# Performance work log

Measured on AMD Instinct MI355X. Metric: run time of the kernel, lower is better.

Reference implementation:

```python
import jax, jax.numpy as jnp
import numpy as np

N, T, D, H = 32, 512, 1024, 1024


def setup_inputs() -> dict:
    key = jax.random.key(0)
    k1, k2, k3, k4 = jax.random.split(key, 4)
    x = jax.random.normal(k1, (N, T, D), jnp.float32)
    prev_ht = jax.random.normal(k2, (N, H), jnp.float32)
    # scale weights to keep sigmoid/tanh out of hard saturation
    weight = jax.random.normal(k3, (D + H, 3 * (D + H)), jnp.float32) / np.sqrt(D + H).astype(np.float32)
    bias = jax.random.normal(k4, (3 * (D + H),), jnp.float32) * 0.1
    return {"x": x, "prev_ht": prev_ht, "weight": weight, "bias": bias}


def _gridgru_forward(x, prev_ht, weight, bias):
    # weight layout per get_weights()
    Wxt = weight[:D, :3 * H]          # (D, 3H)
    Wxd = weight[:D, 3 * H:]          # (D, 3D)
    Whd = weight[D:, 3 * H:]          # (H, 3D)
    Whtg = weight[D:, :2 * H]         # (H, 2H)
    Whtc = weight[D:, 2 * H:3 * H]    # (H, H)
    bt = bias[:3 * H]
    bd = bias[3 * H:]

    # input projection for temporal gates, done once: (N, T, 3H)
    gates = jnp.einsum('ntd,dk->ntk', x, Wxt) + bt

    # temporal GRU recurrence over T (zoneout=0, inference)
    def step(h, g):  # h: (N,H), g: (N,3H)
        gg = jax.nn.sigmoid(g[:, :2 * H] + h @ Whtg)
        u = gg[:, :H]
        r = gg[:, H:]
        hc = jnp.tanh(g[:, 2 * H:] + (r * h) @ Whtc)
        hn = h + u * (hc - h)  # = h - u*h + u*hc
        return hn, hn

    last_ht, ht_t = jax.lax.scan(step, prev_ht, jnp.swapaxes(gates, 0, 1))
    ht = jnp.swapaxes(ht_t, 0, 1)  # (N, T, H)

    # depth-wise gated recurrence (applied per-timestep, no sequential dep)
    grd = jax.nn.sigmoid(bd[:2 * D]
                         + jnp.einsum('ntd,de->nte', x, Wxd[:, :2 * D])
                         + jnp.einsum('nth,he->nte', ht, Whd[:, :2 * D]))
    ud = grd[..., :D]
    rd = grd[..., D:]
    hcd = jnp.tanh(bd[2 * D:]
                   + jnp.einsum('nth,he->nte', ht, Whd[:, 2 * D:])
                   + jnp.einsum('ntd,de->nte', rd * x, Wxd[:, 2 * D:]))
    h = x + ud * (hcd - x)  # = x - ud*x + ud*hcd
    return h, last_ht


def reference(x, prev_ht, weight, bias):
    return _gridgru_forward(x, prev_ht, weight, bias)
```

## Files before the change

### kernel.cpp

```cpp
#include <hip/hip_runtime.h>
#include <stdint.h>

#define T_STEPS 512

typedef short short8 __attribute__((ext_vector_type(8)));
typedef float floatx4 __attribute__((ext_vector_type(4)));
typedef unsigned int u32x4 __attribute__((ext_vector_type(4)));
typedef unsigned int u32x2 __attribute__((ext_vector_type(2)));

#define MFMA16 __builtin_amdgcn_mfma_f32_16x16x32_bf16

__device__ __forceinline__ unsigned short f2bf(float f) {
  unsigned int u = __builtin_bit_cast(unsigned int, f);
  u = u + 0x7fff + ((u >> 16) & 1);
  return (unsigned short)(u >> 16);
}
__device__ __forceinline__ float bf2f(unsigned short s) {
  unsigned int u = ((unsigned int)s) << 16;
  return __builtin_bit_cast(float, u);
}
__device__ __forceinline__ float sigm(float x) { return 1.f / (1.f + __expf(-x)); }
__device__ __forceinline__ float tanh_fast(float x) {
  float e2 = __expf(2.f * x);
  return 1.f - 2.f / (e2 + 1.f);
}

__device__ __forceinline__ void gload16(const void* g, const void* l) {
  __builtin_amdgcn_global_load_lds((const __attribute__((address_space(1))) unsigned int*)g,
                                   (__attribute__((address_space(3))) unsigned int*)l,
                                   16, 0, 0);
}

__device__ __forceinline__ void st_tag(unsigned int* p, unsigned int word) {
  asm volatile("global_store_dword %0, %1, off sc0 sc1" :: "v"(p), "v"(word) : "memory");
}

__device__ __forceinline__ void stage_state(const unsigned int* __restrict__ gsrc,
                                            unsigned int target,
                                            unsigned short* Stg, int tid) {
  const int lane = tid & 63, wave = tid >> 6;
  const unsigned int* src = gsrc + wave * 4096 + lane * 4;
  u32x4 w[16];
  int spins = 0;
  for (;;) {
#pragma unroll
    for (int j = 0; j < 16; ++j)
      asm volatile("global_load_dwordx4 %0, %1, off sc0 sc1"
                   : "=v"(w[j]) : "v"(src + j * 256));
    asm volatile("s_waitcnt vmcnt(0)" ::: "memory");
    __builtin_amdgcn_sched_barrier(0);
    bool ok = true;
#pragma unroll
    for (int j = 0; j < 16; ++j)
#pragma unroll
      for (int q = 0; q < 4; ++q) ok &= ((w[j][q] >> 16) >= target);
    if (__all((int)ok) || ++spins > (1 << 15)) break;
    if (spins > 4) __builtin_amdgcn_s_sleep(1);
  }
  const int half = lane & 1;
  const int chb = lane >> 1;
#pragma unroll
  for (int j = 0; j < 16; ++j) {
    int row = wave * 4 + (j >> 2);
    int c16 = (j & 3) * 32 + chb;
    u32x2 v;
    v[0] = (w[j][0] & 0xffffu) | (w[j][1] << 16);
    v[1] = (w[j][2] & 0xffffu) | (w[j][3] << 16);
    *(u32x2*)((char*)Stg + row * 2048 + ((c16 ^ (row & 7)) * 16) + half * 8) = v;
  }
  __syncthreads();
}

__global__ void pack_bf(const float* __restrict__ in, unsigned short* __restrict__ out, int n) {
  int i = blockIdx.x * 256 + threadIdx.x;
  if (i < n) out[i] = f2bf(in[i]);
}

__global__ void packT(const float* __restrict__ src, int srcStride,
                      unsigned short* __restrict__ dst, int dldk, int koff) {
  __shared__ float tile[32][33];
  int tx = threadIdx.x, ty = threadIdx.y;
  int e0 = blockIdx.x * 32, k0 = blockIdx.y * 32;
#pragma unroll
  for (int i = 0; i < 4; ++i)
    tile[ty + 8 * i][tx] = src[(size_t)(k0 + ty + 8 * i) * srcStride + e0 + tx];
  __syncthreads();
#pragma unroll
  for (int i = 0; i < 4; ++i)
    dst[(size_t)(e0 + ty + 8 * i) * dldk + koff + k0 + tx] = f2bf(tile[tx][ty + 8 * i]);
}

__global__ void sentinel(float* out, float v) { out[0] = v; }

template <int EPI>
__global__ __launch_bounds__(256) void gemm_bt(
    const unsigned short* __restrict__ A0, const unsigned short* __restrict__ A1,
    const unsigned short* __restrict__ BT,
    int M, int Nn, int K, int KA0,
    const float* __restrict__ bias,
    unsigned short* __restrict__ out_bf,
    const float* __restrict__ xf,
    float* __restrict__ ud,
    unsigned short* __restrict__ rdx,
    float* __restrict__ outf) {
  __shared__ unsigned short At[128 * 32];
  __shared__ unsigned short Bt[128 * 32];
  const int tid = threadIdx.x;
  const int lane = tid & 63, wave = tid >> 6;
  const int wm = wave >> 1, wn = wave & 1;
  const int m0 = blockIdx.y * 128, n0 = blockIdx.x * 128;
  const int lr = lane & 15, lk = (lane >> 4) * 8;
  floatx4 acc[4][4] = {};

  for (int k0 = 0; k0 < K; k0 += 32) {
    const unsigned short* As;
    int kk;
    if (k0 < KA0) { As = A0 + (size_t)m0 * KA0 + k0; kk = KA0; }
    else          { As = A1 + (size_t)m0 * (K - KA0) + (k0 - KA0); kk = K - KA0; }
#pragma unroll
    for (int j = 0; j < 2; ++j) {
      int chunk = j * 256 + tid;
      int row = chunk >> 2, kc = chunk & 3;
      gload16(As + (size_t)row * kk + kc * 8, (const char*)At + chunk * 16);
    }
    const unsigned short* Bs = BT + (size_t)n0 * K + k0;
#pragma unroll
    for (int j = 0; j < 2; ++j) {
      int chunk = j * 256 + tid;
      int row = chunk >> 2, kc = chunk & 3;
      gload16(Bs + (size_t)row * K + kc * 8, (const char*)Bt + chunk * 16);
    }
    __syncthreads();
    short8 a[4], b[4];
#pragma unroll
    for (int i = 0; i < 4; ++i) a[i] = *(const short8*)(At + (wm * 64 + i * 16 + lr) * 32 + lk);
#pragma unroll
    for (int i = 0; i < 4; ++i) b[i] = *(const short8*)(Bt + (wn * 64 + i * 16 + lr) * 32 + lk);
#pragma unroll
    for (int i = 0; i < 4; ++i)
#pragma unroll
      for (int j = 0; j < 4; ++j)
        acc[i][j] = MFMA16(a[i], b[j], acc[i][j], 0, 0, 0);
    __syncthreads();
  }

#pragma unroll
  for (int i = 0; i < 4; ++i) {
#pragma unroll
    for (int j = 0; j < 4; ++j) {
      int col = n0 + wn * 64 + j * 16 + lr;
#pragma unroll
      for (int r = 0; r < 4; ++r) {
        int row = m0 + wm * 64 + i * 16 + (lane >> 4) * 4 + r;
        float v = acc[i][j][r];
        if constexpr (EPI == 0) {
          out_bf[(size_t)row * Nn + col] = f2bf(v + bias[col]);
        } else if constexpr (EPI == 1) {
          float s = sigm(v + bias[col]);
          if (col < 1024) {
            ud[(size_t)row * 1024 + col] = s;
          } else {
            size_t ix = (size_t)row * 1024 + (col - 1024);
            rdx[ix] = f2bf(s * xf[ix]);
          }
        } else {
          float hc = tanh_fast(v + bias[col]);
          size_t ix = (size_t)row * 1024 + col;
          float xv = xf[ix];
          outf[ix] = xv + ud[ix] * (hc - xv);
        }
      }
    }
  }
}

__global__ __launch_bounds__(256, 1) void scan_pk(
    const unsigned short* __restrict__ wgT,
    const unsigned short* __restrict__ wcT,
    const unsigned short* __restrict__ gates,
    const float* __restrict__ ph,
    unsigned int* __restrict__ hb32,
    unsigned int* __restrict__ rh32,
    unsigned short* __restrict__ htb,
    float* __restrict__ lastht)
{
  __shared__ unsigned short Wu[16 * 1024];
  __shared__ unsigned short Wr[16 * 1024];
  __shared__ unsigned short Wc[16 * 1024];
  __shared__ unsigned short Stg[16 * 1024];
  __shared__ float Part[8][16][17];

  const int tid = threadIdx.x;
  const int lane = tid & 63, wave = tid >> 6;
  const int lr = lane & 15, lq = lane >> 4;
  const int g = blockIdx.x >> 6, b = blockIdx.x & 63;
  const int row0 = g * 16, col0 = b * 16;
  const int myrow = tid >> 4, myc = tid & 15;

#pragma unroll
  for (int i = 0; i < 8; ++i) {
    int p = i * 256 + tid;
    int wr = p >> 7, kcp = p & 127;
    int kc = kcp ^ (wr & 7);
    gload16(wgT + (size_t)(col0 + wr) * 1024 + kc * 8,        (const char*)Wu + p * 16);
    gload16(wgT + (size_t)(1024 + col0 + wr) * 1024 + kc * 8, (const char*)Wr + p * 16);
    gload16(wcT + (size_t)(col0 + wr) * 1024 + kc * 8,        (const char*)Wc + p * 16);
  }

  float Hl = ph[(size_t)(row0 + myrow) * 1024 + col0 + myc];
  st_tag(&hb32[(size_t)(row0 + myrow) * 1024 + col0 + myc], (1u << 16) | f2bf(Hl));
  __syncthreads();

  const unsigned int* hb32g = hb32 + (size_t)row0 * 1024;
  const unsigned int* rh32g = rh32 + (size_t)row0 * 1024;

  for (int t = 0; t < T_STEPS; ++t) {
    size_t gbase = ((size_t)(row0 + myrow) * T_STEPS + t) * 3072 + col0 + myc;
    unsigned short gU = gates[gbase];
    unsigned short gR = gates[gbase + 1024];
    unsigned short gC = gates[gbase + 2048];

    stage_state(hb32g, (unsigned)(t + 1), Stg, tid);

    {
      floatx4 aR = {};
#pragma unroll
      for (int ks = 0; ks < 8; ++ks) {
        int sw = ((wave * 8 + ks) * 4 + lq) ^ (lr & 7);
        short8 a = *(const short8*)(Stg + lr * 1024 + sw * 8);
        short8 bR = *(const short8*)(Wr + lr * 1024 + sw * 8);
        aR = MFMA16(a, bR, aR, 0, 0, 0);
      }
#pragma unroll
      for (int r = 0; r < 4; ++r) Part[wave][lq * 4 + r][lr] = aR[r];
    }
    __syncthreads();
    {
      float rpre = Part[0][myrow][myc] + Part[1][myrow][myc] +
                   Part[2][myrow][myc] + Part[3][myrow][myc];
      float rv = sigm(rpre + bf2f(gR));
      st_tag(&rh32[(size_t)(row0 + myrow) * 1024 + col0 + myc],
             ((unsigned)(t + 1) << 16) | f2bf(rv * Hl));
    }

    {
      floatx4 aU = {};
#pragma unroll
      for (int ks = 0; ks < 8; ++ks) {
        int sw = ((wave * 8 + ks) * 4 + lq) ^ (lr & 7);
        short8 a = *(const short8*)(Stg + lr * 1024 + sw * 8);
        short8 bU = *(const short8*)(Wu + lr * 1024 + sw * 8);
        aU = MFMA16(a, bU, aU, 0, 0, 0);
      }
#pragma unroll
      for (int r = 0; r < 4; ++r) Part[4 + wave][lq * 4 + r][lr] = aU[r];
    }
    __syncthreads();
    float uv;
    {
      float upre = Part[4][myrow][myc] + Part[5][myrow][myc] +
                   Part[6][myrow][myc] + Part[7][myrow][myc];
      uv = sigm(upre + bf2f(gU));
    }

    stage_state(rh32g, (unsigned)(t + 1), Stg, tid);

    {
      floatx4 c0 = {}, c1 = {};
#pragma unroll
      for (int ks = 0; ks < 8; ks += 2) {
        int sw0 = ((wave * 8 + ks) * 4 + lq) ^ (lr & 7);
        int sw1 = ((wave * 8 + ks + 1) * 4 + lq) ^ (lr & 7);
        short8 a0 = *(const short8*)(Stg + lr * 1024 + sw0 * 8);
        short8 a1 = *(const short8*)(Stg + lr * 1024 + sw1 * 8);
        short8 b0 = *(const short8*)(Wc + lr * 1024 + sw0 * 8);
        short8 b1 = *(const short8*)(Wc + lr * 1024 + sw1 * 8);
        c0 = MFMA16(a0, b0, c0, 0, 0, 0);
        c1 = MFMA16(a1, b1, c1, 0, 0, 0);
      }
#pragma unroll
      for (int r = 0; r < 4; ++r) Part[wave][lq * 4 + r][lr] = c0[r] + c1[r];
    }
    __syncthreads();
    {
      float cpre = Part[0][myrow][myc] + Part[1][myrow][myc] +
                   Part[2][myrow][myc] + Part[3][myrow][myc];
      float hc = tanh_fast(cpre + bf2f(gC));
      float hn = Hl + uv * (hc - Hl);
      Hl = hn;
      unsigned short hv = f2bf(hn);
      st_tag(&hb32[(size_t)(row0 + myrow) * 1024 + col0 + myc],
             ((unsigned)(t + 2) << 16) | hv);
      htb[((size_t)(row0 + myrow) * T_STEPS + t) * 1024 + col0 + myc] = hv;
      if (t == T_STEPS - 1) lastht[(size_t)(row0 + myrow) * 1024 + col0 + myc] = hn;
    }
  }
}

extern "C" void kernel_launch(void* const* d_in, const int* in_sizes, int n_in,
                              void* d_out, int out_size, void* d_ws, size_t ws_size,
                              hipStream_t stream) {
  const float* x    = (const float*)d_in[0];
  const float* ph   = (const float*)d_in[1];
  const float* wgt  = (const float*)d_in[2];
  const float* bias = (const float*)d_in[3];
  float* out = (float*)d_out;

  const size_t SZ_STATE = (size_t)32 * 1024 * 4 * 2;
  const size_t SZ_XBF   = (size_t)16384 * 1024 * 2;
  const size_t SZ_GATES = (size_t)16384 * 3072 * 2;
  const size_t SZ_HTB   = (size_t)16384 * 1024 * 2;
  const size_t SZ_W     = ((size_t)3072 * 1024 + (size_t)2048 * 2048 +
                           (size_t)1024 * 2048 + (size_t)2048 * 1024 +
                           (size_t)1024 * 1024) * 2;
  const size_t REQUIRED = SZ_STATE + SZ_XBF + SZ_GATES + SZ_HTB + SZ_W;

  if (ws_size < REQUIRED) {
    sentinel<<<1, 1, 0, stream>>>(out, (float)ws_size);
    return;
  }

  char* p = (char*)d_ws;
  unsigned int* hb32    = (unsigned int*)p;   p += (size_t)32 * 1024 * 4;
  unsigned int* rh32    = (unsigned int*)p;   p += (size_t)32 * 1024 * 4;
  unsigned short* xbf   = (unsigned short*)p; p += SZ_XBF;
  unsigned short* gates = (unsigned short*)p;
  unsigned short* rdx   = (unsigned short*)p; p += SZ_GATES;
  unsigned short* htb   = (unsigned short*)p; p += SZ_HTB;
  unsigned short* wxtT  = (unsigned short*)p; p += (size_t)3072 * 1024 * 2;
  unsigned short* w1T   = (unsigned short*)p; p += (size_t)2048 * 2048 * 2;
  unsigned short* w2T   = (unsigned short*)p; p += (size_t)1024 * 2048 * 2;
  unsigned short* wgT   = (unsigned short*)p; p += (size_t)2048 * 1024 * 2;
  unsigned short* wcT   = (unsigned short*)p; p += (size_t)1024 * 1024 * 2;
  float* udf = out;

  hipMemsetAsync(hb32, 0, SZ_STATE, stream);

  dim3 tb(32, 8);
  pack_bf<<<65536, 256, 0, stream>>>(x, xbf, 16384 * 1024);
  packT<<<dim3(96, 32), tb, 0, stream>>>(wgt, 6144, wxtT, 1024, 0);
  packT<<<dim3(64, 64), tb, 0, stream>>>(wgt + 3072, 6144, w1T, 2048, 0);
  packT<<<dim3(32, 32), tb, 0, stream>>>(wgt + (size_t)1024 * 6144 + 5120, 6144, w2T, 2048, 0);
  packT<<<dim3(32, 32), tb, 0, stream>>>(wgt + 5120, 6144, w2T, 2048, 1024);
  packT<<<dim3(64, 32), tb, 0, stream>>>(wgt + (size_t)1024 * 6144, 6144, wgT, 1024, 0);
  packT<<<dim3(32, 32), tb, 0, stream>>>(wgt + (size_t)1024 * 6144 + 2048, 6144, wcT, 1024, 0);

  gemm_bt<0><<<dim3(24, 128), 256, 0, stream>>>(xbf, xbf, wxtT, 16384, 3072, 1024, 1024,
                                                bias, gates, nullptr, nullptr, nullptr, nullptr);

  scan_pk<<<128, 256, 0, stream>>>(wgT, wcT, gates, ph, hb32, rh32, htb,
                                   out + (size_t)16384 * 1024);

  gemm_bt<1><<<dim3(16, 128), 256, 0, stream>>>(xbf, htb, w1T, 16384, 2048, 2048, 1024,
                                                bias + 3072, nullptr, x, udf, rdx, nullptr);
  gemm_bt<2><<<dim3(8, 128), 256, 0, stream>>>(htb, rdx, w2T, 16384, 1024, 2048, 1024,
                                               bias + 5120, nullptr, x, udf, nullptr, out);
}
```

Baseline: 3.343 ms.

## Halve scan blocks: each block handles both batch row groups, fuse r/u MFMA passes

Result: slower. 4.547 ms (+36.0%).

```diff
diff --git a/kernel.cpp b/kernel.cpp
--- a/kernel.cpp
+++ b/kernel.cpp
@@ -193,8 +193,7 @@
   const int tid = threadIdx.x;
   const int lane = tid & 63, wave = tid >> 6;
   const int lr = lane & 15, lq = lane >> 4;
-  const int g = blockIdx.x >> 6, b = blockIdx.x & 63;
-  const int row0 = g * 16, col0 = b * 16;
+  const int col0 = blockIdx.x * 16;
   const int myrow = tid >> 4, myc = tid & 15;
 
 #pragma unroll
@@ -207,92 +206,94 @@
     gload16(wcT + (size_t)(col0 + wr) * 1024 + kc * 8,        (const char*)Wc + p * 16);
   }
 
-  float Hl = ph[(size_t)(row0 + myrow) * 1024 + col0 + myc];
-  st_tag(&hb32[(size_t)(row0 + myrow) * 1024 + col0 + myc], (1u << 16) | f2bf(Hl));
+  float HlA = ph[(size_t)myrow * 1024 + col0 + myc];
+  float HlB = ph[(size_t)(16 + myrow) * 1024 + col0 + myc];
+  st_tag(&hb32[(size_t)myrow * 1024 + col0 + myc], (1u << 16) | f2bf(HlA));
+  st_tag(&hb32[(size_t)(16 + myrow) * 1024 + col0 + myc], (1u << 16) | f2bf(HlB));
   __syncthreads();
 
-  const unsigned int* hb32g = hb32 + (size_t)row0 * 1024;
-  const unsigned int* rh32g = rh32 + (size_t)row0 * 1024;
+  const unsigned int* hbA = hb32;
+  const unsigned int* hbB = hb32 + 16 * 1024;
+  const unsigned int* rhA = rh32;
+  const unsigned int* rhB = rh32 + 16 * 1024;
+
+  float uvA, uvB;
 
   for (int t = 0; t < T_STEPS; ++t) {
-    size_t gbase = ((size_t)(row0 + myrow) * T_STEPS + t) * 3072 + col0 + myc;
-    unsigned short gU = gates[gbase];
-    unsigned short gR = gates[gbase + 1024];
-    unsigned short gC = gates[gbase + 2048];
-
-    stage_state(hb32g, (unsigned)(t + 1), Stg, tid);
-
-    {
-      floatx4 aR = {};
-#pragma unroll
-      for (int ks = 0; ks < 8; ++ks) {
-        int sw = ((wave * 8 + ks) * 4 + lq) ^ (lr & 7);
-        short8 a = *(const short8*)(Stg + lr * 1024 + sw * 8);
-        short8 bR = *(const short8*)(Wr + lr * 1024 + sw * 8);
-        aR = MFMA16(a, bR, aR, 0, 0, 0);
-      }
-#pragma unroll
-      for (int r = 0; r < 4; ++r) Part[wave][lq * 4 + r][lr] = aR[r];
-    }
-    __syncthreads();
-    {
-      float rpre = Part[0][myrow][myc] + Part[1][myrow][myc] +
-                   Part[2][myrow][myc] + Part[3][myrow][myc];
-      float rv = sigm(rpre + bf2f(gR));
-      st_tag(&rh32[(size_t)(row0 + myrow) * 1024 + col0 + myc],
-             ((unsigned)(t + 1) << 16) | f2bf(rv * Hl));
-    }
-
-    {
-      floatx4 aU = {};
-#pragma unroll
-      for (int ks = 0; ks < 8; ++ks) {
-        int sw = ((wave * 8 + ks) * 4 + lq) ^ (lr & 7);
-        short8 a = *(const short8*)(Stg + lr * 1024 + sw * 8);
-        short8 bU = *(const short8*)(Wu + lr * 1024 + sw * 8);
-        aU = MFMA16(a, bU, aU, 0, 0, 0);
-      }
-#pragma unroll
-      for (int r = 0; r < 4; ++r) Part[4 + wave][lq * 4 + r][lr] = aU[r];
-    }
-    __syncthreads();
-    float uv;
-    {
-      float upre = Part[4][myrow][myc] + Part[5][myrow][myc] +
-                   Part[6][myrow][myc] + Part[7][myrow][myc];
-      uv = sigm(upre + bf2f(gU));
-    }
-
-    stage_state(rh32g, (unsigned)(t + 1), Stg, tid);
-
-    {
-      floatx4 c0 = {}, c1 = {};
-#pragma unroll
-      for (int ks = 0; ks < 8; ks += 2) {
-        int sw0 = ((wave * 8 + ks) * 4 + lq) ^ (lr & 7);
-        int sw1 = ((wave * 8 + ks + 1) * 4 + lq) ^ (lr & 7);
-        short8 a0 = *(const short8*)(Stg + lr * 1024 + sw0 * 8);
-        short8 a1 = *(const short8*)(Stg + lr * 1024 + sw1 * 8);
-        short8 b0 = *(const short8*)(Wc + lr * 1024 + sw0 * 8);
-        short8 b1 = *(const short8*)(Wc + lr * 1024 + sw1 * 8);
-        c0 = MFMA16(a0, b0, c0, 0, 0, 0);
-        c1 = MFMA16(a1, b1, c1, 0, 0, 0);
-      }
-#pragma unroll
-      for (int r = 0; r < 4; ++r) Part[wave][lq * 4 + r][lr] = c0[r] + c1[r];
-    }
-    __syncthreads();
-    {
-      float cpre = Part[0][myrow][myc] + Part[1][myrow][myc] +
-                   Part[2][myrow][myc] + Part[3][myrow][myc];
-      float hc = tanh_fast(cpre + bf2f(gC));
-      float hn = Hl + uv * (hc - Hl);
-      Hl = hn;
-      unsigned short hv = f2bf(hn);
-      st_tag(&hb32[(size_t)(row0 + myrow) * 1024 + col0 + myc],
-             ((unsigned)(t + 2) << 16) | hv);
-      htb[((size_t)(row0 + myrow) * T_STEPS + t) * 1024 + col0 + myc] = hv;
-      if (t == T_STEPS - 1) lastht[(size_t)(row0 + myrow) * 1024 + col0 + myc] = hn;
+    size_t gbA = ((size_t)myrow * T_STEPS + t) * 3072 + col0 + myc;
+    size_t gbB = ((size_t)(16 + myrow) * T_STEPS + t) * 3072 + col0 + myc;
+    unsigned short gUA = gates[gbA], gRA = gates[gbA + 1024], gCA = gates[gbA + 2048];
+    unsigned short gUB = gates[gbB], gRB = gates[gbB + 1024], gCB = gates[gbB + 2048];
+
+#pragma unroll
+    for (int grp = 0; grp < 2; ++grp) {
+      stage_state(grp ? hbB : hbA, (unsigned)(t + 1), Stg, tid);
+      {
+        floatx4 aR = {}, aU = {};
+#pragma unroll
+        for (int ks = 0; ks < 8; ++ks) {
+          int sw = ((wave * 8 + ks) * 4 + lq) ^ (lr & 7);
+          short8 a = *(const short8*)(Stg + lr * 1024 + sw * 8);
+          short8 bR = *(const short8*)(Wr + lr * 1024 + sw * 8);
+          short8 bU = *(const short8*)(Wu + lr * 1024 + sw * 8);
+          aR = MFMA16(a, bR, aR, 0, 0, 0);
+          aU = MFMA16(a, bU, aU, 0, 0, 0);
+        }
+#pragma unroll
+        for (int r = 0; r < 4; ++r) {
+          Part[wave][lq * 4 + r][lr] = aR[r];
+          Part[4 + wave][lq * 4 + r][lr] = aU[r];
+        }
+      }
+      __syncthreads();
+      {
+        float rpre = Part[0][myrow][myc] + Part[1][myrow][myc] +
+                     Part[2][myrow][myc] + Part[3][myrow][myc];
+        float upre = Part[4][myrow][myc] + Part[5][myrow][myc] +
+                     Part[6][myrow][myc] + Part[7][myrow][myc];
+        float Hl = grp ? HlB : HlA;
+        float rv = sigm(rpre + bf2f(grp ? gRB : gRA));
+        float uv = sigm(upre + bf2f(grp ? gUB : gUA));
+        if (grp) uvB = uv; else uvA = uv;
+        st_tag((unsigned int*)(grp ? rhB : rhA) + (size_t)myrow * 1024 + col0 + myc,
+               ((unsigned)(t + 1) << 16) | f2bf(rv * Hl));
+      }
+    }
+
+#pragma unroll
+    for (int grp = 0; grp < 2; ++grp) {
+      stage_state(grp ? rhB : rhA, (unsigned)(t + 1), Stg, tid);
+      {
+        floatx4 c0 = {}, c1 = {};
+#pragma unroll
+        for (int ks = 0; ks < 8; ks += 2) {
+          int sw0 = ((wave * 8 + ks) * 4 + lq) ^ (lr & 7);
+          int sw1 = ((wave * 8 + ks + 1) * 4 + lq) ^ (lr & 7);
+          short8 a0 = *(const short8*)(Stg + lr * 1024 + sw0 * 8);
+          short8 a1 = *(const short8*)(Stg + lr * 1024 + sw1 * 8);
+          short8 b0 = *(const short8*)(Wc + lr * 1024 + sw0 * 8);
+          short8 b1 = *(const short8*)(Wc + lr * 1024 + sw1 * 8);
+          c0 = MFMA16(a0, b0, c0, 0, 0, 0);
+          c1 = MFMA16(a1, b1, c1, 0, 0, 0);
+        }
+#pragma unroll
+        for (int r = 0; r < 4; ++r) Part[wave][lq * 4 + r][lr] = c0[r] + c1[r];
+      }
+      __syncthreads();
+      {
+        float cpre = Part[0][myrow][myc] + Part[1][myrow][myc] +
+                     Part[2][myrow][myc] + Part[3][myrow][myc];
+        float hc = tanh_fast(cpre + bf2f(grp ? gCB : gCA));
+        float Hl = grp ? HlB : HlA;
+        float uv = grp ? uvB : uvA;
+        float hn = Hl + uv * (hc - Hl);
+        if (grp) HlB = hn; else HlA = hn;
+        unsigned short hv = f2bf(hn);
+        int grow = grp * 16 + myrow;
+        st_tag(&hb32[(size_t)grow * 1024 + col0 + myc], ((unsigned)(t + 2) << 16) | hv);
+        htb[((size_t)grow * T_STEPS + t) * 1024 + col0 + myc] = hv;
+        if (t == T_STEPS - 1) lastht[(size_t)grow * 1024 + col0 + myc] = hn;
+      }
     }
   }
 }
@@ -348,8 +349,8 @@
   gemm_bt<0><<<dim3(24, 128), 256, 0, stream>>>(xbf, xbf, wxtT, 16384, 3072, 1024, 1024,
                                                 bias, gates, nullptr, nullptr, nullptr, nullptr);
 
-  scan_pk<<<128, 256, 0, stream>>>(wgT, wcT, gates, ph, hb32, rh32, htb,
-                                   out + (size_t)16384 * 1024);
+  scan_pk<<<64, 256, 0, stream>>>(wgT, wcT, gates, ph, hb32, rh32, htb,
+                                  out + (size_t)16384 * 1024);
 
   gemm_bt<1><<<dim3(16, 128), 256, 0, stream>>>(xbf, htb, w1T, 16384, 2048, 2048, 1024,
                                                 bias + 3072, nullptr, x, udf, rdx, nullptr);
```

## Retile scan blocks to 8 rows x 32 cols, stream U weights from global

Applied to the files above, without the earlier changes.

After: 4.127 ms. +23.5%, slower.

```diff
diff --git a/kernel.cpp b/kernel.cpp
--- a/kernel.cpp
+++ b/kernel.cpp
@@ -39,19 +39,19 @@
                                             unsigned int target,
                                             unsigned short* Stg, int tid) {
   const int lane = tid & 63, wave = tid >> 6;
-  const unsigned int* src = gsrc + wave * 4096 + lane * 4;
-  u32x4 w[16];
+  const unsigned int* src = gsrc + wave * 2048 + lane * 4;
+  u32x4 w[8];
   int spins = 0;
   for (;;) {
 #pragma unroll
-    for (int j = 0; j < 16; ++j)
+    for (int j = 0; j < 8; ++j)
       asm volatile("global_load_dwordx4 %0, %1, off sc0 sc1"
                    : "=v"(w[j]) : "v"(src + j * 256));
     asm volatile("s_waitcnt vmcnt(0)" ::: "memory");
     __builtin_amdgcn_sched_barrier(0);
     bool ok = true;
 #pragma unroll
-    for (int j = 0; j < 16; ++j)
+    for (int j = 0; j < 8; ++j)
 #pragma unroll
       for (int q = 0; q < 4; ++q) ok &= ((w[j][q] >> 16) >= target);
     if (__all((int)ok) || ++spins > (1 << 15)) break;
@@ -60,8 +60,8 @@
   const int half = lane & 1;
   const int chb = lane >> 1;
 #pragma unroll
-  for (int j = 0; j < 16; ++j) {
-    int row = wave * 4 + (j >> 2);
+  for (int j = 0; j < 8; ++j) {
+    int row = wave * 2 + (j >> 2);
     int c16 = (j & 3) * 32 + chb;
     u32x2 v;
     v[0] = (w[j][0] & 0xffffu) | (w[j][1] << 16);
@@ -184,25 +184,26 @@
     unsigned short* __restrict__ htb,
     float* __restrict__ lastht)
 {
-  __shared__ unsigned short Wu[16 * 1024];
-  __shared__ unsigned short Wr[16 * 1024];
-  __shared__ unsigned short Wc[16 * 1024];
-  __shared__ unsigned short Stg[16 * 1024];
-  __shared__ float Part[8][16][17];
+  __shared__ unsigned short Wr[32 * 1024];
+  __shared__ unsigned short Wc[32 * 1024];
+  __shared__ unsigned short Stg[8 * 1024];
+  __shared__ float PartR[4][8][17];
+  __shared__ float PartU[4][8][17];
 
   const int tid = threadIdx.x;
   const int lane = tid & 63, wave = tid >> 6;
   const int lr = lane & 15, lq = lane >> 4;
-  const int g = blockIdx.x >> 6, b = blockIdx.x & 63;
-  const int row0 = g * 16, col0 = b * 16;
-  const int myrow = tid >> 4, myc = tid & 15;
-
-#pragma unroll
-  for (int i = 0; i < 8; ++i) {
+  const int ch = wave >> 1, kh = wave & 1;
+  const int g = blockIdx.x >> 5, b = blockIdx.x & 31;
+  const int row0 = g * 8, col0 = b * 32;
+  const int myrow = tid >> 5, myc = tid & 31;
+  const int mch = myc >> 4, mcc = myc & 15;
+
+#pragma unroll
+  for (int i = 0; i < 16; ++i) {
     int p = i * 256 + tid;
     int wr = p >> 7, kcp = p & 127;
     int kc = kcp ^ (wr & 7);
-    gload16(wgT + (size_t)(col0 + wr) * 1024 + kc * 8,        (const char*)Wu + p * 16);
     gload16(wgT + (size_t)(1024 + col0 + wr) * 1024 + kc * 8, (const char*)Wr + p * 16);
     gload16(wcT + (size_t)(col0 + wr) * 1024 + kc * 8,        (const char*)Wc + p * 16);
   }
@@ -213,6 +214,7 @@
 
   const unsigned int* hb32g = hb32 + (size_t)row0 * 1024;
   const unsigned int* rh32g = rh32 + (size_t)row0 * 1024;
+  const unsigned short* bub = wgT + (size_t)(col0 + ch * 16 + lr) * 1024 + kh * 512 + lq * 8;
 
   for (int t = 0; t < T_STEPS; ++t) {
     size_t gbase = ((size_t)(row0 + myrow) * T_STEPS + t) * 3072 + col0 + myc;
@@ -223,68 +225,54 @@
     stage_state(hb32g, (unsigned)(t + 1), Stg, tid);
 
     {
-      floatx4 aR = {};
-#pragma unroll
-      for (int ks = 0; ks < 8; ++ks) {
-        int sw = ((wave * 8 + ks) * 4 + lq) ^ (lr & 7);
-        short8 a = *(const short8*)(Stg + lr * 1024 + sw * 8);
-        short8 bR = *(const short8*)(Wr + lr * 1024 + sw * 8);
+      floatx4 aR = {}, aU = {};
+#pragma unroll
+      for (int ks = 0; ks < 16; ++ks) {
+        int sw = ((kh * 16 + ks) * 4 + lq) ^ (lr & 7);
+        short8 a  = *(const short8*)(Stg + (lr & 7) * 1024 + sw * 8);
+        short8 bR = *(const short8*)(Wr + (ch * 16 + lr) * 1024 + sw * 8);
+        short8 bU = *(const short8*)(bub + ks * 32);
         aR = MFMA16(a, bR, aR, 0, 0, 0);
-      }
-#pragma unroll
-      for (int r = 0; r < 4; ++r) Part[wave][lq * 4 + r][lr] = aR[r];
-    }
-    __syncthreads();
-    {
-      float rpre = Part[0][myrow][myc] + Part[1][myrow][myc] +
-                   Part[2][myrow][myc] + Part[3][myrow][myc];
-      float rv = sigm(rpre + bf2f(gR));
-      st_tag(&rh32[(size_t)(row0 + myrow) * 1024 + col0 + myc],
-             ((unsigned)(t + 1) << 16) | f2bf(rv * Hl));
-    }
-
-    {
-      floatx4 aU = {};
-#pragma unroll
-      for (int ks = 0; ks < 8; ++ks) {
-        int sw = ((wave * 8 + ks) * 4 + lq) ^ (lr & 7);
-        short8 a = *(const short8*)(Stg + lr * 1024 + sw * 8);
-        short8 bU = *(const short8*)(Wu + lr * 1024 + sw * 8);
         aU = MFMA16(a, bU, aU, 0, 0, 0);
       }
-#pragma unroll
-      for (int r = 0; r < 4; ++r) Part[4 + wave][lq * 4 + r][lr] = aU[r];
+      if (lq < 2) {
+#pragma unroll
+        for (int r = 0; r < 4; ++r) {
+          PartR[wave][lq * 4 + r][lr] = aR[r];
+          PartU[wave][lq * 4 + r][lr] = aU[r];
+        }
+      }
     }
     __syncthreads();
     float uv;
     {
-      float upre = Part[4][myrow][myc] + Part[5][myrow][myc] +
-                   Part[6][myrow][myc] + Part[7][myrow][myc];
+      float rpre = PartR[mch * 2][myrow][mcc] + PartR[mch * 2 + 1][myrow][mcc];
+      float upre = PartU[mch * 2][myrow][mcc] + PartU[mch * 2 + 1][myrow][mcc];
+      float rv = sigm(rpre + bf2f(gR));
       uv = sigm(upre + bf2f(gU));
+      st_tag(&rh32[(size_t)(row0 + myrow) * 1024 + col0 + myc],
+             ((unsigned)(t + 1) << 16) | f2bf(rv * Hl));
     }
 
     stage_state(rh32g, (unsigned)(t + 1), Stg, tid);
 
     {
-      floatx4 c0 = {}, c1 = {};
-#pragma unroll
-      for (int ks = 0; ks < 8; ks += 2) {
-        int sw0 = ((wave * 8 + ks) * 4 + lq) ^ (lr & 7);
-        int sw1 = ((wave * 8 + ks + 1) * 4 + lq) ^ (lr & 7);
-        short8 a0 = *(const short8*)(Stg + lr * 1024 + sw0 * 8);
-        short8 a1 = *(const short8*)(Stg + lr * 1024 + sw1 * 8);
-        short8 b0 = *(const short8*)(Wc + lr * 1024 + sw0 * 8);
-        short8 b1 = *(const short8*)(Wc + lr * 1024 + sw1 * 8);
-        c0 = MFMA16(a0, b0, c0, 0, 0, 0);
-        c1 = MFMA16(a1, b1, c1, 0, 0, 0);
-      }
-#pragma unroll
-      for (int r = 0; r < 4; ++r) Part[wave][lq * 4 + r][lr] = c0[r] + c1[r];
+      floatx4 c0 = {};
+#pragma unroll
+      for (int ks = 0; ks < 16; ++ks) {
+        int sw = ((kh * 16 + ks) * 4 + lq) ^ (lr & 7);
+        short8 a = *(const short8*)(Stg + (lr & 7) * 1024 + sw * 8);
+        short8 bC = *(const short8*)(Wc + (ch * 16 + lr) * 1024 + sw * 8);
+        c0 = MFMA16(a, bC, c0, 0, 0, 0);
+      }
+      if (lq < 2) {
+#pragma unroll
+        for (int r = 0; r < 4; ++r) PartR[wave][lq * 4 + r][lr] = c0[r];
+      }
     }
     __syncthreads();
     {
-      float cpre = Part[0][myrow][myc] + Part[1][myrow][myc] +
-                   Part[2][myrow][myc] + Part[3][myrow][myc];
+      float cpre = PartR[mch * 2][myrow][mcc] + PartR[mch * 2 + 1][myrow][mcc];
       float hc = tanh_fast(cpre + bf2f(gC));
       float hn = Hl + uv * (hc - Hl);
       Hl = hn;
```
